# Kernel optimization log

Measured on AMD Instinct MI355X. Metric: run time of the kernel, lower is better.

## Reference

```python
import jax, jax.numpy as jnp
import numpy as np

DIM = 4096
N_HEADS = 32
N_KV_HEADS = 8
HEAD_DIM = DIM // N_HEADS  # 128
N_REP = N_HEADS // N_KV_HEADS  # 4
HIDDEN = 14336  # 4*dim -> 2/3 -> *1.3 -> round up to multiple of 256
EPS = 1e-6
BSZ, SEQLEN, CACHE_LEN = 1, 2048, 4096
ROPE_THETA = 500000.0


def setup_inputs() -> dict:
    key = jax.random.key(0)
    ks = jax.random.split(key, 16)
    s = 0.02
    x = jax.random.normal(ks[0], (BSZ, SEQLEN, DIM), jnp.float32)
    cache_k = jax.random.normal(ks[1], (BSZ, CACHE_LEN, N_KV_HEADS, HEAD_DIM), jnp.float32)
    cache_v = jax.random.normal(ks[2], (BSZ, CACHE_LEN, N_KV_HEADS, HEAD_DIM), jnp.float32)
    # causal mask over rolling cache: query i may attend to cache slot j <= (CACHE_LEN - SEQLEN) + i
    qi = jnp.arange(SEQLEN)[:, None]
    kj = jnp.arange(CACHE_LEN)[None, :]
    mask = jnp.where(kj <= (CACHE_LEN - SEQLEN) + qi, 0.0, -1e9).astype(jnp.float32)[None, None]
    # rotary freqs (cos/sin pairs) for the new seqlen positions (start of window here)
    inv = 1.0 / (ROPE_THETA ** (jnp.arange(0, HEAD_DIM, 2, dtype=jnp.float32) / HEAD_DIM))
    t = jnp.arange(SEQLEN, dtype=jnp.float32)
    ang = t[:, None] * inv[None, :]  # [S, HEAD_DIM//2]
    freqs_cis = jnp.stack([jnp.cos(ang), jnp.sin(ang)], axis=-1)  # [S, HD//2, 2]
    # params (stored as (in, out))
    wq = jax.random.normal(ks[3], (DIM, N_HEADS * HEAD_DIM), jnp.float32) * s
    wk = jax.random.normal(ks[4], (DIM, N_KV_HEADS * HEAD_DIM), jnp.float32) * s
    wv = jax.random.normal(ks[5], (DIM, N_KV_HEADS * HEAD_DIM), jnp.float32) * s
    wo = jax.random.normal(ks[6], (N_HEADS * HEAD_DIM, DIM), jnp.float32) * s
    w1 = jax.random.normal(ks[7], (DIM, HIDDEN), jnp.float32) * s
    w2 = jax.random.normal(ks[8], (HIDDEN, DIM), jnp.float32) * s
    w3 = jax.random.normal(ks[9], (DIM, HIDDEN), jnp.float32) * s
    attn_norm_w = jnp.ones((DIM,), jnp.float32)
    ffn_norm_w = jnp.ones((DIM,), jnp.float32)
    return dict(x=x, mask=mask, freqs_cis=freqs_cis, cache_k=cache_k, cache_v=cache_v,
                wq=wq, wk=wk, wv=wv, wo=wo, w1=w1, w2=w2, w3=w3,
                attn_norm_w=attn_norm_w, ffn_norm_w=ffn_norm_w)


def rmsnorm(x, w, eps=EPS):
    return x * jax.lax.rsqrt(jnp.mean(x * x, axis=-1, keepdims=True) + eps) * w


def apply_rope(xq, xk, freqs_cis):
    # xq: [B,S,Hq,D], xk: [B,S,Hkv,D]; freqs_cis: [S, D//2, 2]
    cos = freqs_cis[None, :, None, :, 0]  # [1,S,1,D//2]
    sin = freqs_cis[None, :, None, :, 1]
    def rot(t):
        tp = t.reshape(*t.shape[:-1], -1, 2)
        t0, t1 = tp[..., 0], tp[..., 1]
        o0 = t0 * cos - t1 * sin
        o1 = t0 * sin + t1 * cos
        return jnp.stack([o0, o1], axis=-1).reshape(t.shape)
    return rot(xq), rot(xk)


def reference(x, mask, freqs_cis, cache_k, cache_v, wq, wk, wv, wo, w1, w2, w3, attn_norm_w, ffn_norm_w):
    bsz, seqlen, _ = x.shape
    # --- attention norm ---
    xn = rmsnorm(x, attn_norm_w)
    # --- qkv ---
    xq = (xn @ wq).reshape(bsz, seqlen, N_HEADS, HEAD_DIM)
    xk = (xn @ wk).reshape(bsz, seqlen, N_KV_HEADS, HEAD_DIM)
    xv = (xn @ wv).reshape(bsz, seqlen, N_KV_HEADS, HEAD_DIM)
    xq, xk = apply_rope(xq, xk, freqs_cis)
    # --- rolling KV cache ---
    cache_k = jnp.concatenate([cache_k[:, seqlen:], xk], axis=1)  # [B,CL,Hkv,D]
    cache_v = jnp.concatenate([cache_v[:, seqlen:], xv], axis=1)
    keys = jnp.repeat(cache_k[:bsz], N_REP, axis=2)    # [B,CL,Hq,D]
    values = jnp.repeat(cache_v[:bsz], N_REP, axis=2)
    # --- attention ---
    scores = jnp.einsum('bqhd,bkhd->bhqk', xq, keys) / jnp.sqrt(jnp.float32(HEAD_DIM))
    scores = jax.nn.softmax(scores + mask, axis=-1)
    attn = jnp.einsum('bhqk,bkhd->bqhd', scores, values).reshape(bsz, seqlen, -1)
    h = x + attn @ wo
    # --- ffn (SwiGLU) ---
    hn = rmsnorm(h, ffn_norm_w)
    out = h + (jax.nn.silu(hn @ w1) * (hn @ w3)) @ w2
    return (out, cache_k, cache_v)
```

## Files before the change

### kernel.cpp

```cpp
#include <hip/hip_runtime.h>

typedef _Float16 h16;
typedef _Float16 h16x4 __attribute__((ext_vector_type(4)));
typedef _Float16 h16x8 __attribute__((ext_vector_type(8)));
typedef float f32x4 __attribute__((ext_vector_type(4)));
typedef float f32x16 __attribute__((ext_vector_type(16)));
typedef unsigned short u16;
typedef unsigned long long u64;

__device__ __forceinline__ f32x4 mfma16(h16x8 a, h16x8 b, f32x4 c) {
  return __builtin_amdgcn_mfma_f32_16x16x32_f16(a, b, c, 0, 0, 0);
}
__device__ __forceinline__ f32x16 mfma32(h16x8 a, h16x8 b, f32x16 c) {
  return __builtin_amdgcn_mfma_f32_32x32x16_f16(a, b, c, 0, 0, 0);
}

typedef const __attribute__((address_space(1))) void* gas_p;
typedef __attribute__((address_space(3))) void* las_p;
__device__ __forceinline__ void ldscp16(const void* g, void* l) {
  __builtin_amdgcn_global_load_lds((gas_p)g, (las_p)l, 16, 0, 0);
}
#define VMCNT(n) asm volatile("s_waitcnt vmcnt(" #n ")" ::: "memory")
#define SBAR() asm volatile("s_barrier" ::: "memory")

__global__ __launch_bounds__(256) void rmsnorm_k(
    const float* __restrict__ x, const float* __restrict__ w, h16* __restrict__ out) {
  const int row = blockIdx.x, t = threadIdx.x;
  const float* xr = x + (size_t)row * 4096;
  float4 v[4];
  float ss = 0.f;
#pragma unroll
  for (int j = 0; j < 4; j++) {
    v[j] = *(const float4*)(xr + 4 * t + 1024 * j);
    ss += v[j].x * v[j].x + v[j].y * v[j].y + v[j].z * v[j].z + v[j].w * v[j].w;
  }
#pragma unroll
  for (int off = 1; off < 64; off <<= 1) ss += __shfl_xor(ss, off, 64);
  __shared__ float red[4];
  if ((t & 63) == 0) red[t >> 6] = ss;
  __syncthreads();
  float scale = rsqrtf((red[0] + red[1] + red[2] + red[3]) * (1.f / 4096.f) + 1e-6f);
  h16* orow = out + (size_t)row * 4096;
#pragma unroll
  for (int j = 0; j < 4; j++) {
    float4 wv = *(const float4*)(w + 4 * t + 1024 * j);
    h16x4 o;
    o[0] = (h16)(v[j].x * scale * wv.x);
    o[1] = (h16)(v[j].y * scale * wv.y);
    o[2] = (h16)(v[j].z * scale * wv.z);
    o[3] = (h16)(v[j].w * scale * wv.w);
    *(h16x4*)(orow + 4 * t + 1024 * j) = o;
  }
}

__global__ __launch_bounds__(256) void convw_k(
    const float* __restrict__ W, h16* __restrict__ out, int rowN, int ktiles) {
  __shared__ u16 timg[8192];
  const int t = threadIdx.x, b = blockIdx.x, kt = blockIdx.y;
  const float* src = W + (size_t)(kt * 64) * rowN + b * 128;
#pragma unroll
  for (int i = 0; i < 8; i++) {
    int c = t + (i << 8);
    int krow = c >> 5, nc = (c & 31) << 2;
    float4 v = *(const float4*)(src + (size_t)krow * rowN + nc);
    int kc = krow >> 3, e = krow & 7;
    float vals[4] = {v.x, v.y, v.z, v.w};
#pragma unroll
    for (int j = 0; j < 4; j++) {
      int m = nc + j;
      h16 hv = (h16)vals[j];
      timg[(m << 6) + ((kc ^ (m & 7)) << 3) + e] = __builtin_bit_cast(u16, hv);
    }
  }
  __syncthreads();
  uint4* dst = (uint4*)(out + ((size_t)(b * ktiles + kt) << 13));
  const uint4* s4 = (const uint4*)timg;
#pragma unroll
  for (int i = 0; i < 4; i++) dst[t + (i << 8)] = s4[t + (i << 8)];
}

template <int EPI>
__global__ __launch_bounds__(512, 2) void gemm_k(
    const h16* __restrict__ A, const h16* __restrict__ Wt,
    float* outF, h16* outH, const float* resid, const h16* uin,
    int K, int lda, int ldo, int no0) {
  __shared__ u16 lds[3][24576];
  const int tid = threadIdx.x, lane = tid & 63;
  const int wv = tid >> 6, wr = wv >> 2, wc = wv & 3;
  const int g = lane >> 4, lr = lane & 15;
  const int m0 = blockIdx.y << 7, n0 = blockIdx.x << 8;
  const int ktiles = K >> 6;

  f32x4 acc[4][4];
#pragma unroll
  for (int i = 0; i < 4; i++)
#pragma unroll
    for (int j = 0; j < 4; j++) acc[i][j] = {0.f, 0.f, 0.f, 0.f};

  const int rA = tid >> 3;
  const int kcA = (tid & 7) ^ (rA & 7);
  const h16* gA = A + (size_t)(m0 + rA) * lda + (kcA << 3);
  const h16* gA2 = gA + (size_t)64 * lda;
  const h16* gB0 = Wt + (((size_t)(2 * blockIdx.x) * ktiles) << 13) + tid * 8;
  const h16* gB1 = Wt + (((size_t)(2 * blockIdx.x + 1) * ktiles) << 13) + tid * 8;

  auto issueA = [&](int t) {
    char* base = (char*)lds[t % 3];
    ldscp16(gA + t * 64, base + tid * 16);
    ldscp16(gA2 + t * 64, base + tid * 16 + 8192);
    ldscp16(gB0 + ((size_t)t << 13), base + 16384 + tid * 16);
    ldscp16(gB0 + ((size_t)t << 13) + 4096, base + 16384 + tid * 16 + 8192);
  };
  auto issueB = [&](int t) {
    char* base = (char*)lds[t % 3];
    ldscp16(gB1 + ((size_t)t << 13), base + 32768 + tid * 16);
    ldscp16(gB1 + ((size_t)t << 13) + 4096, base + 32768 + tid * 16 + 8192);
  };

  issueA(0); issueB(0); issueA(1); issueB(1);
  VMCNT(6);
  SBAR();

  for (int t = 0; t < ktiles; ++t) {
    const char* bp = (const char*)lds[t % 3];
    const bool more = (t + 2 < ktiles);
#pragma unroll
    for (int ks = 0; ks < 2; ++ks) {
      h16x8 av[4], bv[4];
      const int cc = (ks << 2) + g;
#pragma unroll
      for (int f = 0; f < 4; f++) {
        int row = (wr << 6) + (f << 4) + lr;
        av[f] = *(const h16x8*)(bp + row * 128 + ((cc ^ (row & 7)) << 4));
        int nr = (wc << 6) + (f << 4) + lr;
        bv[f] = *(const h16x8*)(bp + 16384 + nr * 128 + ((cc ^ (nr & 7)) << 4));
      }
      if (more) {
        if (ks == 0) issueA(t + 2);
        else issueB(t + 2);
      }
      __builtin_amdgcn_s_setprio(1);
#pragma unroll
      for (int fi = 0; fi < 4; fi++)
#pragma unroll
        for (int fj = 0; fj < 4; fj++)
          acc[fi][fj] = mfma16(av[fi], bv[fj], acc[fi][fj]);
      __builtin_amdgcn_s_setprio(0);
    }
    if (t + 1 < ktiles) {
      if (more) VMCNT(6);
      else VMCNT(0);
      SBAR();
    }
  }
#pragma unroll
  for (int fi = 0; fi < 4; fi++) {
    const int row = m0 + (wr << 6) + (fi << 4) + (g << 2);
#pragma unroll
    for (int fj = 0; fj < 4; fj++) {
      const int col = no0 + n0 + (wc << 6) + (fj << 4) + lr;
#pragma unroll
      for (int r = 0; r < 4; r++) {
        float vl = acc[fi][fj][r];
        if constexpr (EPI == 5) {
          if (col < 4096) outH[(size_t)(row + r) * 4096 + col] = (h16)vl;
          else outF[(size_t)(row + r) * 2048 + (col - 4096)] = vl;
        } else {
          size_t idx = (size_t)(row + r) * ldo + col;
          if constexpr (EPI == 1) outH[idx] = (h16)vl;
          else if constexpr (EPI == 2) outF[idx] = resid[idx] + vl;
          else if constexpr (EPI == 3) {
            float u = (float)uin[idx];
            outH[idx] = (h16)((u / (1.f + __expf(-u))) * vl);
          } else outF[idx] = outF[idx] + vl;
        }
      }
    }
  }
}

__global__ __launch_bounds__(256) void rope_q_k(
    const h16* __restrict__ qin, const float* __restrict__ freqs, h16* qout) {
  const int row = blockIdx.x, t = threadIdx.x;
#pragma unroll
  for (int it = 0; it < 8; ++it) {
    int pid = t + 256 * it;
    int head = pid >> 6, pp = pid & 63;
    size_t idx = (size_t)row * 4096 + head * 128 + 2 * pp;
    float x0 = (float)qin[idx], x1 = (float)qin[idx + 1];
    float cs = freqs[row * 128 + 2 * pp], sn = freqs[row * 128 + 2 * pp + 1];
    qout[idx] = (h16)(x0 * cs - x1 * sn);
    qout[idx + 1] = (h16)(x0 * sn + x1 * cs);
  }
}

__global__ __launch_bounds__(256) void cache_build_k(
    const float* __restrict__ oldK, const float* __restrict__ oldV,
    const float* __restrict__ kvraw, const float* __restrict__ freqs,
    float* __restrict__ outK, float* __restrict__ outV,
    h16* __restrict__ Kf, h16* __restrict__ Vt) {
  const int rt = blockIdx.x, kvh = blockIdx.y;
  const int r0 = rt * 64, tid = threadIdx.x;
  __shared__ u16 vtile[64][128];
#pragma unroll
  for (int it = 0; it < 16; ++it) {
    int s = tid + 256 * it;
    int rr = s >> 6, pp = s & 63;
    int r = r0 + rr;
    float k0, k1, v0, v1;
    if (r < 2048) {
      const float* kp = oldK + (size_t)(r + 2048) * 1024 + kvh * 128 + 2 * pp;
      k0 = kp[0]; k1 = kp[1];
      const float* vp = oldV + (size_t)(r + 2048) * 1024 + kvh * 128 + 2 * pp;
      v0 = vp[0]; v1 = vp[1];
    } else {
      int tpos = r - 2048;
      const float* kp = kvraw + (size_t)tpos * 2048 + kvh * 128 + 2 * pp;
      float x0 = kp[0], x1 = kp[1];
      float cs = freqs[tpos * 128 + 2 * pp], sn = freqs[tpos * 128 + 2 * pp + 1];
      k0 = x0 * cs - x1 * sn;
      k1 = x0 * sn + x1 * cs;
      const float* vp = kvraw + (size_t)tpos * 2048 + 1024 + kvh * 128 + 2 * pp;
      v0 = vp[0]; v1 = vp[1];
    }
    size_t oidx = (size_t)r * 1024 + kvh * 128 + 2 * pp;
    outK[oidx] = k0; outK[oidx + 1] = k1;
    outV[oidx] = v0; outV[oidx + 1] = v1;
    size_t kfi = (size_t)kvh * 524288 + (size_t)r * 128 + 2 * pp;
    Kf[kfi] = (h16)k0; Kf[kfi + 1] = (h16)k1;
    h16 h0 = (h16)v0, h1 = (h16)v1;
    vtile[rr][2 * pp] = __builtin_bit_cast(u16, h0);
    vtile[rr][2 * pp + 1] = __builtin_bit_cast(u16, h1);
  }
  __syncthreads();
#pragma unroll
  for (int it = 0; it < 4; ++it) {
    int c = tid + 256 * it;
    int d = c >> 3, rg = c & 7;
    u16 tmp[8];
#pragma unroll
    for (int u = 0; u < 8; u++) tmp[u] = vtile[rg * 8 + u][d];
    *(uint4*)((u16*)Vt + (size_t)kvh * 524288 + (size_t)d * 4096 + r0 + rg * 8) =
        *(uint4*)tmp;
  }
}

__global__ __launch_bounds__(512, 2) void attn_k(
    const h16* __restrict__ Q, const h16* __restrict__ Kf,
    const h16* __restrict__ Vt, h16* __restrict__ O) {
  __shared__ u16 skv[3][16384];
  const int qt = blockIdx.x, h = blockIdx.y;
  const int q0 = qt << 8, kvh = h >> 2;
  const int tid = threadIdx.x, w = tid >> 6, lane = tid & 63;
  const int lq = lane & 31, lh = lane >> 5;
  const h16* Kb = Kf + (size_t)kvh * 524288;
  const h16* Vb = Vt + (size_t)kvh * 524288;
  const int qg = q0 + w * 32 + lq;

  h16x8 qv[8];
  {
    const h16* qp = Q + (size_t)qg * 4096 + h * 128 + (lh << 3);
#pragma unroll
    for (int c = 0; c < 8; c++) qv[c] = *(const h16x8*)(qp + c * 16);
  }
  f32x16 oa[4];
#pragma unroll
  for (int d = 0; d < 4; d++)
#pragma unroll
    for (int v = 0; v < 16; v++) oa[d][v] = 0.f;
  float m2 = -3e38f, l2 = 0.f;
  const int ntiles = 36 + 4 * qt;
  const float sc = 0.08838834764831845f;

  const int jK = tid >> 4, kchK = tid & 15;
  const h16* gK = Kb + (size_t)jK * 128 + ((kchK ^ (jK & 15)) << 3);
  const int dV = tid >> 3, jchV = tid & 7;
  const h16* gV = Vb + (size_t)dV * 4096 + ((jchV ^ (dV & 7)) << 3);

  auto issueK = [&](int jt) {
    char* base = (char*)skv[jt % 3];
    const h16* s = gK + (jt << 6) * 128;
    ldscp16(s, base + tid * 16);
    ldscp16(s + 32 * 128, base + tid * 16 + 8192);
  };
  auto issueV = [&](int jt) {
    char* base = (char*)skv[jt % 3];
    const h16* s = gV + (jt << 6);
    ldscp16(s, base + 16384 + tid * 16);
    ldscp16(s + (size_t)64 * 4096, base + 16384 + tid * 16 + 8192);
  };

  issueK(0); issueV(0); issueK(1); issueV(1);
  VMCNT(4);
  SBAR();

  for (int jt = 0; jt < ntiles; ++jt) {
    const char* bp = (const char*)skv[jt % 3];
    const bool more = (jt + 2 < ntiles);
    if (more) issueK(jt + 2);
    f32x16 st[2];
#pragma unroll
    for (int jb = 0; jb < 2; jb++) {
      f32x16 s;
#pragma unroll
      for (int v = 0; v < 16; v++) s[v] = 0.f;
      const int jr = jb * 32 + lq;
      __builtin_amdgcn_s_setprio(1);
#pragma unroll
      for (int kc = 0; kc < 8; kc++) {
        h16x8 ak =
            *(const h16x8*)(bp + jr * 256 + ((((kc << 1) + lh) ^ (jr & 15)) << 4));
        s = mfma32(ak, qv[kc], s);
      }
      __builtin_amdgcn_s_setprio(0);
      st[jb] = s;
    }
    if (more) issueV(jt + 2);
    const int j0 = jt << 6;
    const bool domask = (jt >= ntiles - 4);
    float pm = -3e38f;
#pragma unroll
    for (int jb = 0; jb < 2; jb++)
#pragma unroll
      for (int v = 0; v < 16; v++) {
        float val = st[jb][v] * sc;
        if (domask) {
          int j = j0 + jb * 32 + (v & 3) + (((v >> 2) & 3) << 3) + (lh << 2);
          if (j > 2048 + qg) val = -1e30f;
        }
        st[jb][v] = val;
        pm = fmaxf(pm, val);
      }
    pm = fmaxf(pm, __shfl_xor(pm, 32, 64));
    if (__any(pm - m2 > 8.f)) {
      float mn = fmaxf(m2, pm);
      float al = __expf(m2 - mn);
      m2 = mn;
      l2 *= al;
#pragma unroll
      for (int d = 0; d < 4; d++) oa[d] *= al;
    }
    float rs = 0.f;
#pragma unroll
    for (int jb = 0; jb < 2; jb++)
#pragma unroll
      for (int v = 0; v < 16; v++) {
        float p = __expf(st[jb][v] - m2);
        st[jb][v] = p;
        rs += p;
      }
    rs += __shfl_xor(rs, 32, 64);
    l2 += rs;
    h16x8 pb[4];
#pragma unroll
    for (int kc = 0; kc < 4; kc++) {
      const int jb = kc >> 1, cb = (kc & 1) << 1;
      const int cs = cb + 1 - lh, ck = cb + lh;
      h16x4 sq, kq;
#pragma unroll
      for (int i = 0; i < 4; i++) {
        sq[i] = (h16)st[jb][(cs << 2) + i];
        kq[i] = (h16)st[jb][(ck << 2) + i];
      }
      u64 rv = __shfl_xor(__builtin_bit_cast(u64, sq), 32, 64);
      h16x4 rq = __builtin_bit_cast(h16x4, rv);
      h16x4 lo = lh ? rq : kq;
      h16x4 hi = lh ? kq : rq;
#pragma unroll
      for (int i = 0; i < 4; i++) {
        pb[kc][i] = lo[i];
        pb[kc][i + 4] = hi[i];
      }
    }
    __builtin_amdgcn_s_setprio(1);
#pragma unroll
    for (int d = 0; d < 4; d++) {
      const int dr = (d << 5) + lq;
#pragma unroll
      for (int kc = 0; kc < 4; kc++) {
        h16x8 av = *(const h16x8*)(bp + 16384 + dr * 128 +
                                   ((((kc << 1) + lh) ^ (dr & 7)) << 4));
        oa[d] = mfma32(av, pb[kc], oa[d]);
      }
    }
    __builtin_amdgcn_s_setprio(0);
    if (jt + 1 < ntiles) {
      if (more) VMCNT(4);
      else VMCNT(0);
      SBAR();
    }
  }
  float rl = 1.f / l2;
  h16* Op = O + (size_t)qg * 4096 + h * 128;
#pragma unroll
  for (int d = 0; d < 4; d++)
#pragma unroll
    for (int b = 0; b < 4; b++) {
      h16x4 ov;
#pragma unroll
      for (int i = 0; i < 4; i++) ov[i] = (h16)(oa[d][(b << 2) + i] * rl);
      *(h16x4*)(Op + (d << 5) + (b << 3) + (lh << 2)) = ov;
    }
}

extern "C" void kernel_launch(void* const* d_in, const int* in_sizes, int n_in,
                              void* d_out, int out_size, void* d_ws, size_t ws_size,
                              hipStream_t stream) {
  const float* x = (const float*)d_in[0];
  const float* freqs = (const float*)d_in[2];
  const float* oldK = (const float*)d_in[3];
  const float* oldV = (const float*)d_in[4];
  const float* wq = (const float*)d_in[5];
  const float* wk = (const float*)d_in[6];
  const float* wvp = (const float*)d_in[7];
  const float* wo = (const float*)d_in[8];
  const float* w1 = (const float*)d_in[9];
  const float* w2 = (const float*)d_in[10];
  const float* w3 = (const float*)d_in[11];
  const float* anw = (const float*)d_in[12];
  const float* fnw = (const float*)d_in[13];
  float* out = (float*)d_out;
  float* outK = out + 8388608;
  float* outV = out + 12582912;

  char* ws = (char*)d_ws;
  h16* xn = (h16*)(ws + 0);
  h16* bufW = (h16*)(ws + 16777216);
  float* hbuf = (float*)(ws + 75497472);
  float* kvraw = (float*)(ws + 75497472);
  h16* kf = (h16*)(ws + 92274688);
  h16* vt = (h16*)(ws + 100663296);
  h16* ub = (h16*)(ws + 109051904);
  h16* qraw = (h16*)(ws + 109051904);
  h16* attnb = (h16*)(ws + 125829120);

  rmsnorm_k<<<2048, 256, 0, stream>>>(x, anw, xn);
  convw_k<<<dim3(32, 64), 256, 0, stream>>>(wq, bufW, 4096, 64);
  convw_k<<<dim3(8, 64), 256, 0, stream>>>(wk, bufW + ((size_t)32 * 64 << 13), 1024, 64);
  convw_k<<<dim3(8, 64), 256, 0, stream>>>(wvp, bufW + ((size_t)40 * 64 << 13), 1024, 64);
  gemm_k<5><<<dim3(24, 16), 512, 0, stream>>>(xn, bufW, kvraw, qraw, nullptr,
                                              nullptr, 4096, 4096, 0, 0);
  rope_q_k<<<2048, 256, 0, stream>>>(qraw, freqs, qraw);
  cache_build_k<<<dim3(64, 8), 256, 0, stream>>>(oldK, oldV, kvraw, freqs, outK,
                                                 outV, kf, vt);
  attn_k<<<dim3(8, 32), 512, 0, stream>>>(qraw, kf, vt, attnb);
  convw_k<<<dim3(32, 64), 256, 0, stream>>>(wo, bufW, 4096, 64);
  gemm_k<2><<<dim3(16, 16), 512, 0, stream>>>(attnb, bufW, hbuf, nullptr, x,
                                              nullptr, 4096, 4096, 4096, 0);
  rmsnorm_k<<<2048, 256, 0, stream>>>(hbuf, fnw, xn);
  convw_k<<<dim3(56, 64), 256, 0, stream>>>(w1, bufW, 14336, 64);
  gemm_k<1><<<dim3(28, 16), 512, 0, stream>>>(xn, bufW, nullptr, ub, nullptr,
                                              nullptr, 4096, 4096, 14336, 0);
  convw_k<<<dim3(56, 64), 256, 0, stream>>>(w1 + 7168, bufW, 14336, 64);
  gemm_k<1><<<dim3(28, 16), 512, 0, stream>>>(xn, bufW, nullptr, ub, nullptr,
                                              nullptr, 4096, 4096, 14336, 7168);
  convw_k<<<dim3(56, 64), 256, 0, stream>>>(w3, bufW, 14336, 64);
  gemm_k<3><<<dim3(28, 16), 512, 0, stream>>>(xn, bufW, nullptr, ub, nullptr, ub,
                                              4096, 4096, 14336, 0);
  convw_k<<<dim3(56, 64), 256, 0, stream>>>(w3 + 7168, bufW, 14336, 64);
  gemm_k<3><<<dim3(28, 16), 512, 0, stream>>>(xn, bufW, nullptr, ub, nullptr, ub,
                                              4096, 4096, 14336, 7168);
  convw_k<<<dim3(32, 112), 256, 0, stream>>>(w2, bufW, 4096, 112);
  gemm_k<2><<<dim3(16, 16), 512, 0, stream>>>(ub, bufW, out, nullptr, hbuf,
                                              nullptr, 7168, 14336, 4096, 0);
  convw_k<<<dim3(32, 112), 256, 0, stream>>>(w2 + (size_t)7168 * 4096, bufW, 4096, 112);
  gemm_k<4><<<dim3(16, 16), 512, 0, stream>>>(ub + 7168, bufW, out, nullptr,
                                              nullptr, nullptr, 7168, 14336, 4096, 0);
}
```

Baseline: 1.710 ms.

## Restructure attention: smaller query tiles, exp2 softmax, MFMA row sums, double buffering

The attention kernel now uses 128-query blocks of 256 threads with a doubled grid, and launches the longest causal tiles first. K/V staging drops from a triple buffer to a double buffer. The softmax scale times log2(e) is folded into Q during RoPE, so the kernel can use exp2 directly without a per-element scale multiply. Probabilities are packed to fp16 with cvt_pkrtz, and the row sums come from an extra MFMA against a ones vector instead of shuffle reductions. The aim is better load balance and less VALU work, at the cost of shallower prefetch and a full vmcnt(0) wait on every tile.

```diff
diff --git a/kernel.cpp b/kernel.cpp
--- a/kernel.cpp
+++ b/kernel.cpp
@@ -3,16 +3,29 @@
 typedef _Float16 h16;
 typedef _Float16 h16x4 __attribute__((ext_vector_type(4)));
 typedef _Float16 h16x8 __attribute__((ext_vector_type(8)));
+typedef __fp16 fp16x2 __attribute__((ext_vector_type(2)));
 typedef float f32x4 __attribute__((ext_vector_type(4)));
 typedef float f32x16 __attribute__((ext_vector_type(16)));
 typedef unsigned short u16;
-typedef unsigned long long u64;
+typedef unsigned int u32;
+typedef unsigned int u32x4 __attribute__((ext_vector_type(4)));
 
 __device__ __forceinline__ f32x4 mfma16(h16x8 a, h16x8 b, f32x4 c) {
   return __builtin_amdgcn_mfma_f32_16x16x32_f16(a, b, c, 0, 0, 0);
 }
 __device__ __forceinline__ f32x16 mfma32(h16x8 a, h16x8 b, f32x16 c) {
   return __builtin_amdgcn_mfma_f32_32x32x16_f16(a, b, c, 0, 0, 0);
+}
+__device__ __forceinline__ float fexp2(float x) {
+#if __has_builtin(__builtin_amdgcn_exp2f)
+  return __builtin_amdgcn_exp2f(x);
+#else
+  return exp2f(x);
+#endif
+}
+__device__ __forceinline__ u32 pkh(float a, float b) {
+  fp16x2 t = __builtin_amdgcn_cvt_pkrtz(a, b);
+  return __builtin_bit_cast(u32, t);
 }
 
 typedef const __attribute__((address_space(1))) void* gas_p;
@@ -182,6 +195,7 @@
 __global__ __launch_bounds__(256) void rope_q_k(
     const h16* __restrict__ qin, const float* __restrict__ freqs, h16* qout) {
   const int row = blockIdx.x, t = threadIdx.x;
+  const float SCL = 0.12751743647239037f;
 #pragma unroll
   for (int it = 0; it < 8; ++it) {
     int pid = t + 256 * it;
@@ -189,8 +203,8 @@
     size_t idx = (size_t)row * 4096 + head * 128 + 2 * pp;
     float x0 = (float)qin[idx], x1 = (float)qin[idx + 1];
     float cs = freqs[row * 128 + 2 * pp], sn = freqs[row * 128 + 2 * pp + 1];
-    qout[idx] = (h16)(x0 * cs - x1 * sn);
-    qout[idx + 1] = (h16)(x0 * sn + x1 * cs);
+    qout[idx] = (h16)((x0 * cs - x1 * sn) * SCL);
+    qout[idx + 1] = (h16)((x0 * sn + x1 * cs) * SCL);
   }
 }
 
@@ -245,12 +259,12 @@
   }
 }
 
-__global__ __launch_bounds__(512, 2) void attn_k(
+__global__ __launch_bounds__(256, 2) void attn_k(
     const h16* __restrict__ Q, const h16* __restrict__ Kf,
     const h16* __restrict__ Vt, h16* __restrict__ O) {
-  __shared__ u16 skv[3][16384];
-  const int qt = blockIdx.x, h = blockIdx.y;
-  const int q0 = qt << 8, kvh = h >> 2;
+  __shared__ u16 skv[2][16384];
+  const int qt = 15 - blockIdx.x, h = blockIdx.y;
+  const int q0 = qt << 7, kvh = h >> 2;
   const int tid = threadIdx.x, w = tid >> 6, lane = tid & 63;
   const int lq = lane & 31, lh = lane >> 5;
   const h16* Kb = Kf + (size_t)kvh * 524288;
@@ -263,41 +277,47 @@
 #pragma unroll
     for (int c = 0; c < 8; c++) qv[c] = *(const h16x8*)(qp + c * 16);
   }
-  f32x16 oa[4];
+  h16x8 hone;
+#pragma unroll
+  for (int i = 0; i < 8; i++) hone[i] = (h16)1.0f;
+  f32x16 oa[4], ol2;
 #pragma unroll
   for (int d = 0; d < 4; d++)
 #pragma unroll
     for (int v = 0; v < 16; v++) oa[d][v] = 0.f;
-  float m2 = -3e38f, l2 = 0.f;
-  const int ntiles = 36 + 4 * qt;
-  const float sc = 0.08838834764831845f;
-
-  const int jK = tid >> 4, kchK = tid & 15;
-  const h16* gK = Kb + (size_t)jK * 128 + ((kchK ^ (jK & 15)) << 3);
-  const int dV = tid >> 3, jchV = tid & 7;
-  const h16* gV = Vb + (size_t)dV * 4096 + ((jchV ^ (dV & 7)) << 3);
+#pragma unroll
+  for (int v = 0; v < 16; v++) ol2[v] = 0.f;
+  float m2 = -3e38f;
+  const int ntiles = 34 + 2 * qt;
+
+  const int jK = tid >> 4, kch = tid & 15;
+  const h16* gK = Kb + (size_t)jK * 128 + ((kch ^ (jK & 15)) << 3);
+  const int dV = tid >> 3, jch = tid & 7;
+  const h16* gV = Vb + (size_t)dV * 4096 + ((jch ^ (dV & 7)) << 3);
 
   auto issueK = [&](int jt) {
-    char* base = (char*)skv[jt % 3];
-    const h16* s = gK + (jt << 6) * 128;
-    ldscp16(s, base + tid * 16);
-    ldscp16(s + 32 * 128, base + tid * 16 + 8192);
+    char* base = (char*)skv[jt & 1];
+    const h16* s = gK + (size_t)(jt << 6) * 128;
+#pragma unroll
+    for (int i = 0; i < 4; i++)
+      ldscp16(s + (size_t)i * 2048, base + tid * 16 + i * 4096);
   };
   auto issueV = [&](int jt) {
-    char* base = (char*)skv[jt % 3];
+    char* base = (char*)skv[jt & 1] + 16384;
     const h16* s = gV + (jt << 6);
-    ldscp16(s, base + 16384 + tid * 16);
-    ldscp16(s + (size_t)64 * 4096, base + 16384 + tid * 16 + 8192);
+#pragma unroll
+    for (int i = 0; i < 4; i++)
+      ldscp16(s + (size_t)i * 131072, base + tid * 16 + i * 4096);
   };
 
-  issueK(0); issueV(0); issueK(1); issueV(1);
-  VMCNT(4);
+  issueK(0); issueV(0);
+  VMCNT(0);
   SBAR();
 
   for (int jt = 0; jt < ntiles; ++jt) {
-    const char* bp = (const char*)skv[jt % 3];
-    const bool more = (jt + 2 < ntiles);
-    if (more) issueK(jt + 2);
+    const char* bp = (const char*)skv[jt & 1];
+    const bool more = (jt + 1 < ntiles);
+    if (more) issueK(jt + 1);
     f32x16 st[2];
 #pragma unroll
     for (int jb = 0; jb < 2; jb++) {
@@ -315,62 +335,53 @@
       __builtin_amdgcn_s_setprio(0);
       st[jb] = s;
     }
-    if (more) issueV(jt + 2);
-    const int j0 = jt << 6;
-    const bool domask = (jt >= ntiles - 4);
-    float pm = -3e38f;
-#pragma unroll
-    for (int jb = 0; jb < 2; jb++)
-#pragma unroll
-      for (int v = 0; v < 16; v++) {
-        float val = st[jb][v] * sc;
-        if (domask) {
+    if (more) issueV(jt + 1);
+    if (jt >= ntiles - 2) {
+      const int j0 = jt << 6;
+#pragma unroll
+      for (int jb = 0; jb < 2; jb++)
+#pragma unroll
+        for (int v = 0; v < 16; v++) {
           int j = j0 + jb * 32 + (v & 3) + (((v >> 2) & 3) << 3) + (lh << 2);
-          if (j > 2048 + qg) val = -1e30f;
+          if (j > 2048 + qg) st[jb][v] = -1e30f;
         }
-        st[jb][v] = val;
-        pm = fmaxf(pm, val);
-      }
+    }
+    float pm = fmaxf(st[0][0], st[0][1]);
+#pragma unroll
+    for (int v = 2; v < 16; v += 2) pm = fmaxf(fmaxf(st[0][v], st[0][v + 1]), pm);
+#pragma unroll
+    for (int v = 0; v < 16; v += 2) pm = fmaxf(fmaxf(st[1][v], st[1][v + 1]), pm);
     pm = fmaxf(pm, __shfl_xor(pm, 32, 64));
     if (__any(pm - m2 > 8.f)) {
       float mn = fmaxf(m2, pm);
-      float al = __expf(m2 - mn);
+      float al = fexp2(m2 - mn);
       m2 = mn;
-      l2 *= al;
 #pragma unroll
       for (int d = 0; d < 4; d++) oa[d] *= al;
-    }
-    float rs = 0.f;
+      ol2 *= al;
+    }
+    u32 pw[2][8];
 #pragma unroll
     for (int jb = 0; jb < 2; jb++)
 #pragma unroll
-      for (int v = 0; v < 16; v++) {
-        float p = __expf(st[jb][v] - m2);
-        st[jb][v] = p;
-        rs += p;
-      }
-    rs += __shfl_xor(rs, 32, 64);
-    l2 += rs;
+      for (int c = 0; c < 4; c++) {
+        float p0 = fexp2(st[jb][4 * c] - m2);
+        float p1 = fexp2(st[jb][4 * c + 1] - m2);
+        float p2 = fexp2(st[jb][4 * c + 2] - m2);
+        float p3 = fexp2(st[jb][4 * c + 3] - m2);
+        pw[jb][2 * c] = pkh(p0, p1);
+        pw[jb][2 * c + 1] = pkh(p2, p3);
+      }
     h16x8 pb[4];
 #pragma unroll
     for (int kc = 0; kc < 4; kc++) {
       const int jb = kc >> 1, cb = (kc & 1) << 1;
-      const int cs = cb + 1 - lh, ck = cb + lh;
-      h16x4 sq, kq;
-#pragma unroll
-      for (int i = 0; i < 4; i++) {
-        sq[i] = (h16)st[jb][(cs << 2) + i];
-        kq[i] = (h16)st[jb][(ck << 2) + i];
-      }
-      u64 rv = __shfl_xor(__builtin_bit_cast(u64, sq), 32, 64);
-      h16x4 rq = __builtin_bit_cast(h16x4, rv);
-      h16x4 lo = lh ? rq : kq;
-      h16x4 hi = lh ? kq : rq;
-#pragma unroll
-      for (int i = 0; i < 4; i++) {
-        pb[kc][i] = lo[i];
-        pb[kc][i + 4] = hi[i];
-      }
+      u32 oa_ = pw[jb][2 * cb], ob_ = pw[jb][2 * cb + 1];
+      u32 oc_ = pw[jb][2 * cb + 2], od_ = pw[jb][2 * cb + 3];
+      u32 s0 = lh ? oa_ : oc_, s1 = lh ? ob_ : od_;
+      u32 r0 = __shfl_xor(s0, 32, 64), r1 = __shfl_xor(s1, 32, 64);
+      u32x4 wds = {lh ? r0 : oa_, lh ? r1 : ob_, lh ? oc_ : r0, lh ? od_ : r1};
+      pb[kc] = __builtin_bit_cast(h16x8, wds);
     }
     __builtin_amdgcn_s_setprio(1);
 #pragma unroll
@@ -383,14 +394,15 @@
         oa[d] = mfma32(av, pb[kc], oa[d]);
       }
     }
+#pragma unroll
+    for (int kc = 0; kc < 4; kc++) ol2 = mfma32(hone, pb[kc], ol2);
     __builtin_amdgcn_s_setprio(0);
-    if (jt + 1 < ntiles) {
-      if (more) VMCNT(4);
-      else VMCNT(0);
+    if (more) {
+      VMCNT(0);
       SBAR();
     }
   }
-  float rl = 1.f / l2;
+  float rl = 1.f / ol2[0];
   h16* Op = O + (size_t)qg * 4096 + h * 128;
 #pragma unroll
   for (int d = 0; d < 4; d++)
@@ -443,7 +455,7 @@
   rope_q_k<<<2048, 256, 0, stream>>>(qraw, freqs, qraw);
   cache_build_k<<<dim3(64, 8), 256, 0, stream>>>(oldK, oldV, kvraw, freqs, outK,
                                                  outV, kf, vt);
-  attn_k<<<dim3(8, 32), 512, 0, stream>>>(qraw, kf, vt, attnb);
+  attn_k<<<dim3(16, 32), 256, 0, stream>>>(qraw, kf, vt, attnb);
   convw_k<<<dim3(32, 64), 256, 0, stream>>>(wo, bufW, 4096, 64);
   gemm_k<2><<<dim3(16, 16), 512, 0, stream>>>(attnb, bufW, hbuf, nullptr, x,
                                               nullptr, 4096, 4096, 4096, 0);
```

After: 1.533 ms. 1.12x faster.
